# Kernel tuning notes

Measured on AMD Instinct MI355X. Metric: run time of the kernel, lower is better.

## Reference

```python
import jax, jax.numpy as jnp
import numpy as np

EPS = 1e-12  # matches torch F.normalize eps


def _gradients(img):
    # forward differences along D, H, W with last slice zeroed (via zero-pad)
    dx = jnp.pad(img[:, :, 1:] - img[:, :, :-1], ((0, 0), (0, 0), (0, 1), (0, 0), (0, 0)))
    dy = jnp.pad(img[:, :, :, 1:] - img[:, :, :, :-1], ((0, 0), (0, 0), (0, 0), (0, 1), (0, 0)))
    dz = jnp.pad(img[:, :, :, :, 1:] - img[:, :, :, :, :-1], ((0, 0), (0, 0), (0, 0), (0, 0), (0, 1)))
    return dx, dy, dz


def _cos(f, t, axis):
    # cosine similarity along `axis` with torch-normalize eps semantics
    fn = f / jnp.maximum(jnp.linalg.norm(f, axis=axis, keepdims=True), EPS)
    tn = t / jnp.maximum(jnp.linalg.norm(t, axis=axis, keepdims=True), EPS)
    return jnp.sum(fn * tn, axis=axis)


def _sploss(f, t, ax_row, ax_col):
    # trace(norm_rows(F) @ norm_rows(T)^T) == sum of row cosine sims; same for cols.
    bc = f.shape[0] * f.shape[1]
    a = jnp.sum(_cos(f, t, ax_col)) / (f.shape[ax_row] * bc)
    b = jnp.sum(_cos(f, t, ax_row)) / (f.shape[ax_col] * bc)
    return -(a + b)


def setup_inputs() -> dict:
    key = jax.random.key(0)
    k1, k2 = jax.random.split(key)
    shape = (2, 1, 160, 160, 160)  # [B, C, D, H, W]
    fake = jax.random.normal(k1, shape, dtype=jnp.float32)
    true = jax.random.normal(k2, shape, dtype=jnp.float32)
    return {"fake": fake, "true": true}


def reference(fake, true):
    fx, fy, fz = _gradients(fake)
    tx, ty, tz = _gradients(true)
    # dim='x' slices are [H, W] -> rows axis 3, cols axis 4
    trace_x = _sploss(fx, tx, 3, 4)
    # dim='y' slices are [D, W] -> rows axis 2, cols axis 4
    trace_y = _sploss(fy, ty, 2, 4)
    # dim='z' slices are [D, H] -> rows axis 2, cols axis 3
    trace_z = _sploss(fz, tz, 2, 3)
    return (trace_x + trace_y + trace_z) / 3.0
```

## Files before the change

### kernel.cpp

```cpp
#include <hip/hip_runtime.h>
#include <math.h>

#define DD 160
#define HH 160
#define WW 160
#define NB 2
#define SLICE (HH * WW)
#define NV 51200
#define NVTOT (4 * NV)
#define NC 5
#define RPC 32
#define NIT 4
#define NTHR 320

static constexpr float EPS = 1e-12f;
static constexpr float SCALE = -1.0f / 960.0f;

#define ELEM(v, j) ((j) == 0 ? (v).x : ((j) == 1 ? (v).y : ((j) == 2 ? (v).z : (v).w)))

__global__ void zero_kernel(float* out) {
  if (threadIdx.x == 0) out[0] = 0.0f;
}

__global__ __launch_bounds__(NTHR) void mainAB(const float* __restrict__ f,
                                               const float* __restrict__ t,
                                               float* __restrict__ P,
                                               float* __restrict__ out) {
  __shared__ float sd[8960];
  __shared__ float red[32][6];
  __shared__ float cpad[32];
  const int tid = threadIdx.x;
  const int l = tid % 40;
  const int g = tid / 40;
  const int w = 4 * l;
  const int wn = (w + 4 < WW) ? (w + 4) : (WW - 1);
  const int blk = blockIdx.x;

  if ((blk & 1) == 0) {
    const int id = blk >> 1;
    const int hc = id % NC;
    const int bd = id / NC;
    const int d = bd % DD;
    const size_t base = (size_t)bd * SLICE;
    const float* fp = f + base;
    const float* tp = t + base;
    const int dstep = (d < DD - 1) ? SLICE : 0;
    float ah[24];
#pragma unroll
    for (int c = 0; c < 24; ++c) ah[c] = 0.0f;

#pragma unroll
    for (int it = 0; it < NIT; ++it) {
      const int rl = it * 8 + g;
      const int h = hc * RPC + rl;
      const int hstep = (h < HH - 1) ? WW : 0;
      const float* rf = fp + h * WW;
      const float* rt = tp + h * WW;
      const float4 F0 = *(const float4*)(rf + w);
      const float4 T0 = *(const float4*)(rt + w);
      const float4 FD = *(const float4*)(rf + dstep + w);
      const float4 TD = *(const float4*)(rt + dstep + w);
      const float4 FH = *(const float4*)(rf + hstep + w);
      const float4 TH = *(const float4*)(rt + hstep + w);
      const float fz = rf[wn], tz = rt[wn];
      float xd = 0, xf = 0, xt = 0, yd = 0, yf = 0, yt = 0;
#pragma unroll
      for (int j = 0; j < 4; ++j) {
        const float f0 = ELEM(F0, j), t0 = ELEM(T0, j);
        const float gxf = ELEM(FD, j) - f0, gxt = ELEM(TD, j) - t0;
        const float gyf = ELEM(FH, j) - f0, gyt = ELEM(TH, j) - t0;
        const float fnx = (j < 3) ? ELEM(F0, j + 1) : fz;
        const float tnx = (j < 3) ? ELEM(T0, j + 1) : tz;
        const float gzf = fnx - f0, gzt = tnx - t0;
        xd += gxf * gxt; xf += gxf * gxf; xt += gxt * gxt;
        yd += gyf * gyt; yf += gyf * gyf; yt += gyt * gyt;
        ah[j * 6 + 0] += gxf * gxt; ah[j * 6 + 1] += gxf * gxf; ah[j * 6 + 2] += gxt * gxt;
        ah[j * 6 + 3] += gzf * gzt; ah[j * 6 + 4] += gzf * gzf; ah[j * 6 + 5] += gzt * gzt;
      }
      float* s = &sd[(rl * 40 + l) * 7];
      s[0] = xd; s[1] = xf; s[2] = xt; s[3] = yd; s[4] = yf; s[5] = yt;
    }
    __syncthreads();
    if (tid < 192) {
      const int row = tid / 6, c = tid % 6;
      float s = 0.0f;
#pragma unroll 8
      for (int ll = 0; ll < 40; ++ll) s += sd[(row * 40 + ll) * 7 + c];
      red[row][c] = s;
    }
    __syncthreads();
    if (tid < 32) {
      const float cx = red[tid][0] / (fmaxf(sqrtf(red[tid][1]), EPS) * fmaxf(sqrtf(red[tid][2]), EPS));
      const float cy = red[tid][3] / (fmaxf(sqrtf(red[tid][4]), EPS) * fmaxf(sqrtf(red[tid][5]), EPS));
      cpad[tid] = cx + cy;
    }
    float* s3 = &sd[(g * 40 + l) * 25];
#pragma unroll
    for (int c = 0; c < 24; ++c) s3[c] = ah[c];
    __syncthreads();
    if (tid == 0) {
      float s = 0.0f;
#pragma unroll
      for (int i = 0; i < 32; ++i) s += cpad[i];
      atomicAdd(out, s * SCALE);
    }
    for (int task = tid; task < 960; task += NTHR) {
      const int ll = task / 24, c = task % 24;
      float s = 0.0f;
#pragma unroll
      for (int gg = 0; gg < 8; ++gg) s += sd[(gg * 40 + ll) * 25 + c];
      const int j = c / 6, cc = c % 6;
      const int wi = 4 * ll + j;
      const size_t vec = (cc < 3) ? (size_t)(bd * 160 + wi) : (size_t)(NV + bd * 160 + wi);
      P[((size_t)hc * NVTOT + vec) * 3 + (cc % 3)] = s;
    }
  } else {
    const int id = blk >> 1;
    const int dc = id % NC;
    const int bh = id / NC;
    const int b = bh / HH;
    const int h = bh % HH;
    const size_t base = (size_t)b * DD * SLICE + (size_t)h * WW;
    const float* fp = f + base;
    const float* tp = t + base;
    const int hstep = (h < HH - 1) ? WW : 0;
    float ad[24];
#pragma unroll
    for (int c = 0; c < 24; ++c) ad[c] = 0.0f;

#pragma unroll
    for (int it = 0; it < NIT; ++it) {
      const int dloc = dc * RPC + it * 8 + g;
      const float* rf = fp + (size_t)dloc * SLICE;
      const float* rt = tp + (size_t)dloc * SLICE;
      const float4 F0 = *(const float4*)(rf + w);
      const float4 T0 = *(const float4*)(rt + w);
      const float4 FH = *(const float4*)(rf + hstep + w);
      const float4 TH = *(const float4*)(rt + hstep + w);
      const float fz = rf[wn], tz = rt[wn];
#pragma unroll
      for (int j = 0; j < 4; ++j) {
        const float f0 = ELEM(F0, j), t0 = ELEM(T0, j);
        const float gyf = ELEM(FH, j) - f0, gyt = ELEM(TH, j) - t0;
        const float fnx = (j < 3) ? ELEM(F0, j + 1) : fz;
        const float tnx = (j < 3) ? ELEM(T0, j + 1) : tz;
        const float gzf = fnx - f0, gzt = tnx - t0;
        ad[j * 6 + 0] += gyf * gyt; ad[j * 6 + 1] += gyf * gyf; ad[j * 6 + 2] += gyt * gyt;
        ad[j * 6 + 3] += gzf * gzt; ad[j * 6 + 4] += gzf * gzf; ad[j * 6 + 5] += gzt * gzt;
      }
    }
    float* s3 = &sd[(g * 40 + l) * 25];
#pragma unroll
    for (int c = 0; c < 24; ++c) s3[c] = ad[c];
    __syncthreads();
    for (int task = tid; task < 960; task += NTHR) {
      const int ll = task / 24, c = task % 24;
      float s = 0.0f;
#pragma unroll
      for (int gg = 0; gg < 8; ++gg) s += sd[(gg * 40 + ll) * 25 + c];
      const int j = c / 6, cc = c % 6;
      const int wi = 4 * ll + j;
      const size_t vec = (cc < 3) ? (size_t)(2 * NV + bh * 160 + wi) : (size_t)(3 * NV + bh * 160 + wi);
      P[((size_t)dc * NVTOT + vec) * 3 + (cc % 3)] = s;
    }
  }
}

__global__ __launch_bounds__(256) void finalize_kernel(const float* __restrict__ P,
                                                       float* __restrict__ out) {
  const int v = blockIdx.x * 256 + threadIdx.x;
  float c = 0.0f;
  if (v < NVTOT) {
    float dot = 0.0f, ff = 0.0f, tt = 0.0f;
#pragma unroll
    for (int ch = 0; ch < NC; ++ch) {
      const size_t o = ((size_t)ch * NVTOT + v) * 3;
      dot += P[o]; ff += P[o + 1]; tt += P[o + 2];
    }
    c = dot / (fmaxf(sqrtf(ff), EPS) * fmaxf(sqrtf(tt), EPS));
  }
#pragma unroll
  for (int m = 32; m >= 1; m >>= 1) c += __shfl_xor(c, m);
  __shared__ float part[4];
  if ((threadIdx.x & 63) == 0) part[threadIdx.x >> 6] = c;
  __syncthreads();
  if (threadIdx.x == 0) atomicAdd(out, (part[0] + part[1] + part[2] + part[3]) * SCALE);
}

extern "C" void kernel_launch(void* const* d_in, const int* in_sizes, int n_in,
                              void* d_out, int out_size, void* d_ws, size_t ws_size,
                              hipStream_t stream) {
  const float* fk = (const float*)d_in[0];
  const float* tr = (const float*)d_in[1];
  float* out = (float*)d_out;
  float* P = (float*)d_ws;

  hipLaunchKernelGGL(zero_kernel, dim3(1), dim3(64), 0, stream, out);
  hipLaunchKernelGGL(mainAB, dim3(2 * NB * DD * NC), dim3(NTHR), 0, stream, fk, tr, P, out);
  hipLaunchKernelGGL(finalize_kernel, dim3((NVTOT + 255) / 256), dim3(256), 0, stream, P, out);
}
```

Baseline: 151.6 us.

## Map rows to whole wavefronts and reduce per-row sums with shuffles

Measured after the change: 148.5 us. 2.0% less time.

```diff
diff --git a/kernel.cpp b/kernel.cpp
--- a/kernel.cpp
+++ b/kernel.cpp
@@ -10,8 +10,9 @@
 #define NVTOT (4 * NV)
 #define NC 5
 #define RPC 32
-#define NIT 4
-#define NTHR 320
+#define RPW 8
+#define NTHR 256
+#define NWAVE 4
 
 static constexpr float EPS = 1e-12f;
 static constexpr float SCALE = -1.0f / 960.0f;
@@ -22,22 +23,30 @@
   if (threadIdx.x == 0) out[0] = 0.0f;
 }
 
-__global__ __launch_bounds__(NTHR) void mainAB(const float* __restrict__ f,
-                                               const float* __restrict__ t,
-                                               float* __restrict__ P,
-                                               float* __restrict__ out) {
-  __shared__ float sd[8960];
-  __shared__ float red[32][6];
-  __shared__ float cpad[32];
+__global__ __launch_bounds__(NTHR, 4) void mainAB(const float* __restrict__ f,
+                                                  const float* __restrict__ t,
+                                                  float* __restrict__ P,
+                                                  float* __restrict__ out) {
+  __shared__ float sd[NWAVE * 40 * 25];
+  __shared__ float cpad[NWAVE];
   const int tid = threadIdx.x;
-  const int l = tid % 40;
-  const int g = tid / 40;
-  const int w = 4 * l;
+  const int wv = tid >> 6;
+  const int l = tid & 63;
+  const bool act = (l < 40);
+  const int w = act ? 4 * l : 156;
   const int wn = (w + 4 < WW) ? (w + 4) : (WW - 1);
   const int blk = blockIdx.x;
+  const bool roleA = ((blk & 1) == 0);
+  const int id = blk >> 1;
 
-  if ((blk & 1) == 0) {
-    const int id = blk >> 1;
+  float acc[24];
+#pragma unroll
+  for (int c = 0; c < 24; ++c) acc[c] = 0.0f;
+
+  int vbase1, vbase2, ch;
+  float accCos = 0.0f;
+
+  if (roleA) {
     const int hc = id % NC;
     const int bd = id / NC;
     const int d = bd % DD;
@@ -45,124 +54,113 @@
     const float* fp = f + base;
     const float* tp = t + base;
     const int dstep = (d < DD - 1) ? SLICE : 0;
-    float ah[24];
+    const int h0 = hc * RPC + wv * RPW;
+    vbase1 = bd * 160;
+    vbase2 = NV + bd * 160;
+    ch = hc;
+
+    float4 F0, T0;
+    if (act) {
+      F0 = *(const float4*)(fp + h0 * WW + w);
+      T0 = *(const float4*)(tp + h0 * WW + w);
+    }
 #pragma unroll
-    for (int c = 0; c < 24; ++c) ah[c] = 0.0f;
-
-#pragma unroll
-    for (int it = 0; it < NIT; ++it) {
-      const int rl = it * 8 + g;
-      const int h = hc * RPC + rl;
+    for (int it = 0; it < RPW; ++it) {
+      const int h = h0 + it;
       const int hstep = (h < HH - 1) ? WW : 0;
       const float* rf = fp + h * WW;
       const float* rt = tp + h * WW;
-      const float4 F0 = *(const float4*)(rf + w);
-      const float4 T0 = *(const float4*)(rt + w);
-      const float4 FD = *(const float4*)(rf + dstep + w);
-      const float4 TD = *(const float4*)(rt + dstep + w);
-      const float4 FH = *(const float4*)(rf + hstep + w);
-      const float4 TH = *(const float4*)(rt + hstep + w);
-      const float fz = rf[wn], tz = rt[wn];
       float xd = 0, xf = 0, xt = 0, yd = 0, yf = 0, yt = 0;
+      if (act) {
+        const float4 FD = *(const float4*)(rf + dstep + w);
+        const float4 TD = *(const float4*)(rt + dstep + w);
+        const float4 F1 = *(const float4*)(rf + hstep + w);
+        const float4 T1 = *(const float4*)(rt + hstep + w);
+        const float fz = rf[wn], tz = rt[wn];
 #pragma unroll
-      for (int j = 0; j < 4; ++j) {
-        const float f0 = ELEM(F0, j), t0 = ELEM(T0, j);
-        const float gxf = ELEM(FD, j) - f0, gxt = ELEM(TD, j) - t0;
-        const float gyf = ELEM(FH, j) - f0, gyt = ELEM(TH, j) - t0;
-        const float fnx = (j < 3) ? ELEM(F0, j + 1) : fz;
-        const float tnx = (j < 3) ? ELEM(T0, j + 1) : tz;
-        const float gzf = fnx - f0, gzt = tnx - t0;
-        xd += gxf * gxt; xf += gxf * gxf; xt += gxt * gxt;
-        yd += gyf * gyt; yf += gyf * gyf; yt += gyt * gyt;
-        ah[j * 6 + 0] += gxf * gxt; ah[j * 6 + 1] += gxf * gxf; ah[j * 6 + 2] += gxt * gxt;
-        ah[j * 6 + 3] += gzf * gzt; ah[j * 6 + 4] += gzf * gzf; ah[j * 6 + 5] += gzt * gzt;
+        for (int j = 0; j < 4; ++j) {
+          const float f0 = ELEM(F0, j), t0 = ELEM(T0, j);
+          const float gxf = ELEM(FD, j) - f0, gxt = ELEM(TD, j) - t0;
+          const float gyf = ELEM(F1, j) - f0, gyt = ELEM(T1, j) - t0;
+          const float fnx = (j < 3) ? ELEM(F0, j + 1) : fz;
+          const float tnx = (j < 3) ? ELEM(T0, j + 1) : tz;
+          const float gzf = fnx - f0, gzt = tnx - t0;
+          xd += gxf * gxt; xf += gxf * gxf; xt += gxt * gxt;
+          yd += gyf * gyt; yf += gyf * gyf; yt += gyt * gyt;
+          acc[j * 6 + 0] += gxf * gxt; acc[j * 6 + 1] += gxf * gxf; acc[j * 6 + 2] += gxt * gxt;
+          acc[j * 6 + 3] += gzf * gzt; acc[j * 6 + 4] += gzf * gzf; acc[j * 6 + 5] += gzt * gzt;
+        }
+        F0 = F1; T0 = T1;
       }
-      float* s = &sd[(rl * 40 + l) * 7];
-      s[0] = xd; s[1] = xf; s[2] = xt; s[3] = yd; s[4] = yf; s[5] = yt;
-    }
-    __syncthreads();
-    if (tid < 192) {
-      const int row = tid / 6, c = tid % 6;
-      float s = 0.0f;
-#pragma unroll 8
-      for (int ll = 0; ll < 40; ++ll) s += sd[(row * 40 + ll) * 7 + c];
-      red[row][c] = s;
-    }
-    __syncthreads();
-    if (tid < 32) {
-      const float cx = red[tid][0] / (fmaxf(sqrtf(red[tid][1]), EPS) * fmaxf(sqrtf(red[tid][2]), EPS));
-      const float cy = red[tid][3] / (fmaxf(sqrtf(red[tid][4]), EPS) * fmaxf(sqrtf(red[tid][5]), EPS));
-      cpad[tid] = cx + cy;
-    }
-    float* s3 = &sd[(g * 40 + l) * 25];
 #pragma unroll
-    for (int c = 0; c < 24; ++c) s3[c] = ah[c];
-    __syncthreads();
-    if (tid == 0) {
-      float s = 0.0f;
-#pragma unroll
-      for (int i = 0; i < 32; ++i) s += cpad[i];
-      atomicAdd(out, s * SCALE);
-    }
-    for (int task = tid; task < 960; task += NTHR) {
-      const int ll = task / 24, c = task % 24;
-      float s = 0.0f;
-#pragma unroll
-      for (int gg = 0; gg < 8; ++gg) s += sd[(gg * 40 + ll) * 25 + c];
-      const int j = c / 6, cc = c % 6;
-      const int wi = 4 * ll + j;
-      const size_t vec = (cc < 3) ? (size_t)(bd * 160 + wi) : (size_t)(NV + bd * 160 + wi);
-      P[((size_t)hc * NVTOT + vec) * 3 + (cc % 3)] = s;
+      for (int m = 1; m <= 32; m <<= 1) {
+        xd += __shfl_xor(xd, m); xf += __shfl_xor(xf, m); xt += __shfl_xor(xt, m);
+        yd += __shfl_xor(yd, m); yf += __shfl_xor(yf, m); yt += __shfl_xor(yt, m);
+      }
+      if (l == 0) {
+        accCos += xd / (fmaxf(sqrtf(xf), EPS) * fmaxf(sqrtf(xt), EPS));
+        accCos += yd / (fmaxf(sqrtf(yf), EPS) * fmaxf(sqrtf(yt), EPS));
+      }
     }
   } else {
-    const int id = blk >> 1;
     const int dc = id % NC;
     const int bh = id / NC;
     const int b = bh / HH;
     const int h = bh % HH;
-    const size_t base = (size_t)b * DD * SLICE + (size_t)h * WW;
-    const float* fp = f + base;
-    const float* tp = t + base;
+    const float* fp = f + (size_t)b * DD * SLICE + (size_t)h * WW;
+    const float* tp = t + (size_t)b * DD * SLICE + (size_t)h * WW;
     const int hstep = (h < HH - 1) ? WW : 0;
-    float ad[24];
-#pragma unroll
-    for (int c = 0; c < 24; ++c) ad[c] = 0.0f;
+    const int d0 = dc * RPC + wv * RPW;
+    vbase1 = 2 * NV + bh * 160;
+    vbase2 = 3 * NV + bh * 160;
+    ch = dc;
 
 #pragma unroll
-    for (int it = 0; it < NIT; ++it) {
-      const int dloc = dc * RPC + it * 8 + g;
-      const float* rf = fp + (size_t)dloc * SLICE;
-      const float* rt = tp + (size_t)dloc * SLICE;
-      const float4 F0 = *(const float4*)(rf + w);
-      const float4 T0 = *(const float4*)(rt + w);
-      const float4 FH = *(const float4*)(rf + hstep + w);
-      const float4 TH = *(const float4*)(rt + hstep + w);
-      const float fz = rf[wn], tz = rt[wn];
+    for (int it = 0; it < RPW; ++it) {
+      const float* rf = fp + (size_t)(d0 + it) * SLICE;
+      const float* rt = tp + (size_t)(d0 + it) * SLICE;
+      if (act) {
+        const float4 F0 = *(const float4*)(rf + w);
+        const float4 T0 = *(const float4*)(rt + w);
+        const float4 FH = *(const float4*)(rf + hstep + w);
+        const float4 TH = *(const float4*)(rt + hstep + w);
+        const float fz = rf[wn], tz = rt[wn];
 #pragma unroll
-      for (int j = 0; j < 4; ++j) {
-        const float f0 = ELEM(F0, j), t0 = ELEM(T0, j);
-        const float gyf = ELEM(FH, j) - f0, gyt = ELEM(TH, j) - t0;
-        const float fnx = (j < 3) ? ELEM(F0, j + 1) : fz;
-        const float tnx = (j < 3) ? ELEM(T0, j + 1) : tz;
-        const float gzf = fnx - f0, gzt = tnx - t0;
-        ad[j * 6 + 0] += gyf * gyt; ad[j * 6 + 1] += gyf * gyf; ad[j * 6 + 2] += gyt * gyt;
-        ad[j * 6 + 3] += gzf * gzt; ad[j * 6 + 4] += gzf * gzf; ad[j * 6 + 5] += gzt * gzt;
+        for (int j = 0; j < 4; ++j) {
+          const float f0 = ELEM(F0, j), t0 = ELEM(T0, j);
+          const float gyf = ELEM(FH, j) - f0, gyt = ELEM(TH, j) - t0;
+          const float fnx = (j < 3) ? ELEM(F0, j + 1) : fz;
+          const float tnx = (j < 3) ? ELEM(T0, j + 1) : tz;
+          const float gzf = fnx - f0, gzt = tnx - t0;
+          acc[j * 6 + 0] += gyf * gyt; acc[j * 6 + 1] += gyf * gyf; acc[j * 6 + 2] += gyt * gyt;
+          acc[j * 6 + 3] += gzf * gzt; acc[j * 6 + 4] += gzf * gzf; acc[j * 6 + 5] += gzt * gzt;
+        }
       }
     }
-    float* s3 = &sd[(g * 40 + l) * 25];
+  }
+
+  if (act) {
+    float* s = &sd[(wv * 40 + l) * 25];
 #pragma unroll
-    for (int c = 0; c < 24; ++c) s3[c] = ad[c];
-    __syncthreads();
-    for (int task = tid; task < 960; task += NTHR) {
-      const int ll = task / 24, c = task % 24;
-      float s = 0.0f;
+    for (int c = 0; c < 24; ++c) s[c] = acc[c];
+  }
+  if (roleA && l == 0) cpad[wv] = accCos;
+  __syncthreads();
+  if (roleA && tid == 0)
+    atomicAdd(out, (cpad[0] + cpad[1] + cpad[2] + cpad[3]) * SCALE);
+
+  if (tid < 160) {
+    const int ll = tid >> 2, j = tid & 3;
+    float s[6];
 #pragma unroll
-      for (int gg = 0; gg < 8; ++gg) s += sd[(gg * 40 + ll) * 25 + c];
-      const int j = c / 6, cc = c % 6;
-      const int wi = 4 * ll + j;
-      const size_t vec = (cc < 3) ? (size_t)(2 * NV + bh * 160 + wi) : (size_t)(3 * NV + bh * 160 + wi);
-      P[((size_t)dc * NVTOT + vec) * 3 + (cc % 3)] = s;
+    for (int c = 0; c < 6; ++c) {
+      s[c] = sd[(0 * 40 + ll) * 25 + j * 6 + c] + sd[(1 * 40 + ll) * 25 + j * 6 + c]
+           + sd[(2 * 40 + ll) * 25 + j * 6 + c] + sd[(3 * 40 + ll) * 25 + j * 6 + c];
     }
+    const size_t o1 = ((size_t)ch * NVTOT + (vbase1 + tid)) * 3;
+    const size_t o2 = ((size_t)ch * NVTOT + (vbase2 + tid)) * 3;
+    P[o1 + 0] = s[0]; P[o1 + 1] = s[1]; P[o1 + 2] = s[2];
+    P[o2 + 0] = s[3]; P[o2 + 1] = s[4]; P[o2 + 2] = s[5];
   }
 }
 
```
